# Performance work log

Hardware: AMD Instinct MI355X
Metric: run time of the kernel (lower is better)

## Reference

```python
import jax, jax.numpy as jnp
import numpy as np

B, T, K = 512, 1024, 48          # batch, seq_len, n_tokens
START, END = 46, 47              # token_dict['START'], token_dict['END']
NEG = -10000.0


def setup_inputs() -> dict:
    key = jax.random.key(0)
    k1, k2 = jax.random.split(key)
    feats = jax.random.normal(k1, (B, T, K), dtype=jnp.float32)
    transitions = jax.random.normal(k2, (K, K), dtype=jnp.float32)
    return {"feats": feats, "transitions": transitions}


def _mask_transitions(transitions):
    # Mirrors __init__: no transition out of END-column target / into START row.
    t = transitions.at[START, :].set(NEG)
    t = t.at[:, END].set(NEG)
    return t


def _crf_logz(feats, trans):
    """forward_prop: CRF forward algorithm. feats [T,K], trans [K_next,K_prev]."""
    init = jnp.full((K,), NEG, feats.dtype).at[START].set(0.0)

    def step(alpha, feat):
        # scores[next, prev] = alpha[prev] + trans[next, prev] + feat[next]
        scores = alpha[None, :] + trans + feat[:, None]
        return jax.nn.logsumexp(scores, axis=1), None

    alpha, _ = jax.lax.scan(step, init, feats)
    return jax.nn.logsumexp(alpha + trans[END])


def _viterbi(feats, trans):
    """viterbi_decode: max-product recurrence + backtrace. feats [T,K]."""
    init = jnp.full((K,), NEG, feats.dtype).at[START].set(0.0)

    def step(v, feat):
        # NOTE: original takes argmax BEFORE adding emission, then adds feat.
        scores = v[None, :] + trans          # [K_next, K_prev]
        bp = jnp.argmax(scores, axis=1)      # backpointers [K]
        return jnp.max(scores, axis=1) + feat, bp

    v, bptrs = jax.lax.scan(step, init, feats)   # bptrs [T, K]
    term = v + trans[END]
    last = jnp.argmax(term)
    path_score = term[last]

    def back(tag, bp):
        return bp[tag], tag

    _, path = jax.lax.scan(back, last, bptrs, reverse=True)  # path [T]
    return path_score, path


def reference(feats, transitions):
    trans = _mask_transitions(transitions)
    logz = jax.vmap(lambda f: _crf_logz(f, trans))(feats)          # [B]
    scores, paths = jax.vmap(lambda f: _viterbi(f, trans))(feats)  # [B], [B,T]
    return logz, scores, paths
```

## Files before the change

kernel.cpp:

```cpp
#include <hip/hip_runtime.h>

#define NB 512
#define NT 1024
#define NK 48
#define NEGV -10000.0f
#define S_START 46
#define S_END 47

__device__ __forceinline__ float rfl_f32(float x) {
    return __int_as_float(__builtin_amdgcn_readfirstlane(__float_as_int(x)));
}

extern "C" __global__ __launch_bounds__(128, 1)
void crf_fused(const float* __restrict__ feats, const float* __restrict__ trans,
               float* __restrict__ out)
{
    __shared__ unsigned char bp[NT * NK];
    __shared__ unsigned char comp[64 * NK];
    __shared__ unsigned char boundary[64];
    __shared__ float eabuf[64];
    __shared__ float vbuf[64];

    const int b = blockIdx.x;
    const int wave = threadIdx.x >> 6;
    const int lane = threadIdx.x & 63;
    const bool act = lane < NK;
    const int LL = act ? lane : (NK - 1);
    const float* f = feats + (size_t)b * NT * NK;
    const float* fb = f + LL;

    float tEnd = NEGV;
    if (act && lane != S_END) tEnd = trans[S_END * NK + lane];

    if (wave == 0) {
        float Erow[NK];
        {
            const bool rowdead = (lane == S_START);
            const float4* r4 = (const float4*)(trans + LL * NK);
            #pragma unroll
            for (int q = 0; q < NK / 4; ++q) {
                float4 r = r4[q];
                const int c = 4 * q;
                Erow[c + 0] = (rowdead || c + 0 == S_END) ? 0.0f : __expf(r.x);
                Erow[c + 1] = (rowdead || c + 1 == S_END) ? 0.0f : __expf(r.y);
                Erow[c + 2] = (rowdead || c + 2 == S_END) ? 0.0f : __expf(r.z);
                Erow[c + 3] = (rowdead || c + 3 == S_END) ? 0.0f : __expf(r.w);
            }
        }
        float u = (lane == S_START) ? 0.0f : NEGV;
        float Muni = 0.0f;
        eabuf[lane] = __expf(u);
        __builtin_amdgcn_wave_barrier();

        float fr0 = fb[0 * NK], fr1 = fb[1 * NK], fr2 = fb[2 * NK], fr3 = fb[3 * NK];

        auto fstep = [&](float fc) {
            float ea[NK];
            {
                const float4* e4 = (const float4*)eabuf;
                #pragma unroll
                for (int q = 0; q < NK / 4; ++q) {
                    float4 r = e4[q];
                    ea[4 * q + 0] = r.x; ea[4 * q + 1] = r.y;
                    ea[4 * q + 2] = r.z; ea[4 * q + 3] = r.w;
                }
            }
            float a0 = 0.f, a1 = 0.f, a2 = 0.f, a3 = 0.f;
            #pragma unroll
            for (int p = 0; p < NK; p += 4) {
                a0 = fmaf(Erow[p + 0], ea[p + 0], a0);
                a1 = fmaf(Erow[p + 1], ea[p + 1], a1);
                a2 = fmaf(Erow[p + 2], ea[p + 2], a2);
                a3 = fmaf(Erow[p + 3], ea[p + 3], a3);
            }
            float acc = (a0 + a1) + (a2 + a3);
            float w = __logf(acc) + fc;
            float dM = rfl_f32(w);
            Muni += dM;
            u = w - dM;
            __builtin_amdgcn_wave_barrier();
            eabuf[lane] = __expf(u);
            __builtin_amdgcn_wave_barrier();
        };

        for (int t = 0; t < NT; t += 4) {
            { float fc = fr0; int nr = (t + 4 < NT) ? t + 4 : NT - 1; fr0 = fb[nr * NK]; fstep(fc); }
            { float fc = fr1; int nr = (t + 5 < NT) ? t + 5 : NT - 1; fr1 = fb[nr * NK]; fstep(fc); }
            { float fc = fr2; int nr = (t + 6 < NT) ? t + 6 : NT - 1; fr2 = fb[nr * NK]; fstep(fc); }
            { float fc = fr3; int nr = (t + 7 < NT) ? t + 7 : NT - 1; fr3 = fb[nr * NK]; fstep(fc); }
        }
        float x = act ? (u + tEnd) : -INFINITY;
        float M2 = x;
        #pragma unroll
        for (int off = 32; off >= 1; off >>= 1)
            M2 = fmaxf(M2, __shfl_xor(M2, off, 64));
        float e = __expf(x - M2);
        #pragma unroll
        for (int off = 32; off >= 1; off >>= 1)
            e += __shfl_xor(e, off, 64);
        if (lane == 0) out[b] = Muni + M2 + __logf(e);
    } else {
        float trow[NK];
        {
            const bool rowdead = (lane == S_START);
            const float4* r4 = (const float4*)(trans + LL * NK);
            #pragma unroll
            for (int q = 0; q < NK / 4; ++q) {
                float4 r = r4[q];
                const int c = 4 * q;
                trow[c + 0] = (rowdead || c + 0 == S_END) ? NEGV : r.x;
                trow[c + 1] = (rowdead || c + 1 == S_END) ? NEGV : r.y;
                trow[c + 2] = (rowdead || c + 2 == S_END) ? NEGV : r.z;
                trow[c + 3] = (rowdead || c + 3 == S_END) ? NEGV : r.w;
            }
        }
        float v = (lane == S_START) ? 0.0f : NEGV;
        vbuf[lane] = v;
        __builtin_amdgcn_wave_barrier();

        float fr0 = fb[0 * NK], fr1 = fb[1 * NK], fr2 = fb[2 * NK], fr3 = fb[3 * NK];
        const int big = 63;

        auto vstep = [&](float fc, int tt) {
            float s[NK];
            {
                const float4* v4 = (const float4*)vbuf;
                #pragma unroll
                for (int q = 0; q < NK / 4; ++q) {
                    float4 r = v4[q];
                    s[4 * q + 0] = r.x + trow[4 * q + 0];
                    s[4 * q + 1] = r.y + trow[4 * q + 1];
                    s[4 * q + 2] = r.z + trow[4 * q + 2];
                    s[4 * q + 3] = r.w + trow[4 * q + 3];
                }
            }
            float m16[16];
            #pragma unroll
            for (int i = 0; i < 16; ++i)
                m16[i] = fmaxf(fmaxf(s[3 * i], s[3 * i + 1]), s[3 * i + 2]);
            float m6[6];
            #pragma unroll
            for (int i = 0; i < 5; ++i)
                m6[i] = fmaxf(fmaxf(m16[3 * i], m16[3 * i + 1]), m16[3 * i + 2]);
            m6[5] = m16[15];
            float best = fmaxf(fmaxf(fmaxf(m6[0], m6[1]), m6[2]),
                               fmaxf(fmaxf(m6[3], m6[4]), m6[5]));
            int ix[NK];
            #pragma unroll
            for (int p = 0; p < NK; ++p)
                ix[p] = (s[p] != best) ? big : p;
            int n16[16];
            #pragma unroll
            for (int i = 0; i < 16; ++i)
                n16[i] = min(min(ix[3 * i], ix[3 * i + 1]), ix[3 * i + 2]);
            int n6[6];
            #pragma unroll
            for (int i = 0; i < 5; ++i)
                n6[i] = min(min(n16[3 * i], n16[3 * i + 1]), n16[3 * i + 2]);
            n6[5] = n16[15];
            int bi = min(min(min(n6[0], n6[1]), n6[2]),
                         min(min(n6[3], n6[4]), n6[5]));

            bp[tt * NK + LL] = (unsigned char)bi;
            v = best + fc;
            __builtin_amdgcn_wave_barrier();
            vbuf[lane] = v;
            __builtin_amdgcn_wave_barrier();
        };

        for (int t = 0; t < NT; t += 4) {
            { float fc = fr0; int nr = (t + 4 < NT) ? t + 4 : NT - 1; fr0 = fb[nr * NK]; vstep(fc, t + 0); }
            { float fc = fr1; int nr = (t + 5 < NT) ? t + 5 : NT - 1; fr1 = fb[nr * NK]; vstep(fc, t + 1); }
            { float fc = fr2; int nr = (t + 6 < NT) ? t + 6 : NT - 1; fr2 = fb[nr * NK]; vstep(fc, t + 2); }
            { float fc = fr3; int nr = (t + 7 < NT) ? t + 7 : NT - 1; fr3 = fb[nr * NK]; vstep(fc, t + 3); }
        }
        float xv = act ? (v + tEnd) : -INFINITY;
        int idx = act ? lane : 63;
        float val = xv;
        #pragma unroll
        for (int off = 32; off >= 1; off >>= 1) {
            float ov = __shfl_xor(val, off, 64);
            int   oi = __shfl_xor(idx, off, 64);
            if (ov > val || (ov == val && oi < idx)) { val = ov; idx = oi; }
        }
        if (lane == 0) out[NB + b] = val;
        const int last = idx;

        __builtin_amdgcn_wave_barrier();
        int cur[NK];
        #pragma unroll
        for (int k = 0; k < NK; ++k) cur[k] = k;
        const int tbase = lane * 16;
        for (int i = 15; i >= 0; --i) {
            const int t = tbase + i;
            #pragma unroll
            for (int k = 0; k < NK; ++k) cur[k] = bp[t * NK + cur[k]];
        }
        #pragma unroll
        for (int k = 0; k < NK; ++k) comp[lane * NK + k] = (unsigned char)cur[k];
        __builtin_amdgcn_wave_barrier();

        if (lane == 0) {
            int tag = last;
            for (int l = 63; l >= 0; --l) {
                boundary[l] = (unsigned char)tag;
                tag = comp[l * NK + tag];
            }
        }
        __builtin_amdgcn_wave_barrier();

        int tag = boundary[lane];
        float* pout = out + 2 * NB + (size_t)b * NT;
        for (int i = 15; i >= 0; --i) {
            const int t = tbase + i;
            pout[t] = (float)tag;
            tag = bp[t * NK + tag];
        }
    }
}

extern "C" void kernel_launch(void* const* d_in, const int* in_sizes, int n_in,
                              void* d_out, int out_size, void* d_ws, size_t ws_size,
                              hipStream_t stream) {
    (void)in_sizes; (void)n_in; (void)d_ws; (void)ws_size; (void)out_size;
    const float* feats = (const float*)d_in[0];
    const float* trans = (const float*)d_in[1];
    float* out = (float*)d_out;
    crf_fused<<<dim3(NB), dim3(128), 0, stream>>>(feats, trans, out);
}
```

Before: 519.0 us.

## Split Viterbi into max-only sweep, parallel chunk recompute, and trace kernels

The sequential Viterbi sweep now computes only the running max, with no argmax, and checkpoints the score vector every 16 steps to workspace. A second kernel launched over (batch, chunk) recomputes backpointers for each chunk from its checkpoint in parallel and writes them, plus a composed chunk map, to global memory. A third kernel chains the chunk maps and backtraces the path. The goal is to shorten the serial critical path of the Viterbi wave, at the cost of extra launches and workspace traffic. The old fused kernel remains as a fallback when workspace is missing or too small.

```diff
diff --git a/kernel.cpp b/kernel.cpp
--- a/kernel.cpp
+++ b/kernel.cpp
@@ -6,18 +6,27 @@
 #define NEGV -10000.0f
 #define S_START 46
 #define S_END 47
+#define NCH 64
+#define CLEN 16
+
+#define WS_CKPT 0
+#define WS_CKPT_SZ (NB * NCH * NK * 4)
+#define WS_LAST (WS_CKPT + WS_CKPT_SZ)
+#define WS_LAST_SZ (NB * 4)
+#define WS_COMP (WS_LAST + WS_LAST_SZ)
+#define WS_COMP_SZ (NB * NCH * NK)
+#define WS_BP (WS_COMP + WS_COMP_SZ)
+#define WS_BP_SZ (NB * NCH * CLEN * NK)
+#define WS_NEED (WS_BP + WS_BP_SZ)
 
 __device__ __forceinline__ float rfl_f32(float x) {
     return __int_as_float(__builtin_amdgcn_readfirstlane(__float_as_int(x)));
 }
 
 extern "C" __global__ __launch_bounds__(128, 1)
-void crf_fused(const float* __restrict__ feats, const float* __restrict__ trans,
-               float* __restrict__ out)
+void crf_sweep(const float* __restrict__ feats, const float* __restrict__ trans,
+               float* __restrict__ out, unsigned char* __restrict__ ws)
 {
-    __shared__ unsigned char bp[NT * NK];
-    __shared__ unsigned char comp[64 * NK];
-    __shared__ unsigned char boundary[64];
     __shared__ float eabuf[64];
     __shared__ float vbuf[64];
 
@@ -117,9 +126,10 @@
         float v = (lane == S_START) ? 0.0f : NEGV;
         vbuf[lane] = v;
         __builtin_amdgcn_wave_barrier();
+        float* ckpt = (float*)(ws + WS_CKPT) + (size_t)b * NCH * NK;
+        if (act) ckpt[lane] = v;
 
         float fr0 = fb[0 * NK], fr1 = fb[1 * NK], fr2 = fb[2 * NK], fr3 = fb[3 * NK];
-        const int big = 63;
 
         auto vstep = [&](float fc, int tt) {
             float s[NK];
@@ -145,6 +155,309 @@
             m6[5] = m16[15];
             float best = fmaxf(fmaxf(fmaxf(m6[0], m6[1]), m6[2]),
                                fmaxf(fmaxf(m6[3], m6[4]), m6[5]));
+            v = best + fc;
+            __builtin_amdgcn_wave_barrier();
+            vbuf[lane] = v;
+            __builtin_amdgcn_wave_barrier();
+            if (((tt + 1) & (CLEN - 1)) == 0 && (tt + 1) < NT && act)
+                ckpt[((tt + 1) >> 4) * NK + lane] = v;
+        };
+
+        for (int t = 0; t < NT; t += 4) {
+            { float fc = fr0; int nr = (t + 4 < NT) ? t + 4 : NT - 1; fr0 = fb[nr * NK]; vstep(fc, t + 0); }
+            { float fc = fr1; int nr = (t + 5 < NT) ? t + 5 : NT - 1; fr1 = fb[nr * NK]; vstep(fc, t + 1); }
+            { float fc = fr2; int nr = (t + 6 < NT) ? t + 6 : NT - 1; fr2 = fb[nr * NK]; vstep(fc, t + 2); }
+            { float fc = fr3; int nr = (t + 7 < NT) ? t + 7 : NT - 1; fr3 = fb[nr * NK]; vstep(fc, t + 3); }
+        }
+        float xv = act ? (v + tEnd) : -INFINITY;
+        int idx = act ? lane : 63;
+        float val = xv;
+        #pragma unroll
+        for (int off = 32; off >= 1; off >>= 1) {
+            float ov = __shfl_xor(val, off, 64);
+            int   oi = __shfl_xor(idx, off, 64);
+            if (ov > val || (ov == val && oi < idx)) { val = ov; idx = oi; }
+        }
+        if (lane == 0) {
+            out[NB + b] = val;
+            ((int*)(ws + WS_LAST))[b] = idx;
+        }
+    }
+}
+
+extern "C" __global__ void
+crf_chunks(const float* __restrict__ feats, const float* __restrict__ trans,
+           unsigned char* __restrict__ ws)
+{
+    __shared__ float vbuf[64];
+    __shared__ unsigned char bp16[CLEN * NK];
+
+    const int b = blockIdx.x;
+    const int c = blockIdx.y;
+    const int lane = threadIdx.x & 63;
+    const bool act = lane < NK;
+    const int LL = act ? lane : (NK - 1);
+
+    float trow[NK];
+    {
+        const bool rowdead = (lane == S_START);
+        const float4* r4 = (const float4*)(trans + LL * NK);
+        #pragma unroll
+        for (int q = 0; q < NK / 4; ++q) {
+            float4 r = r4[q];
+            const int cc = 4 * q;
+            trow[cc + 0] = (rowdead || cc + 0 == S_END) ? NEGV : r.x;
+            trow[cc + 1] = (rowdead || cc + 1 == S_END) ? NEGV : r.y;
+            trow[cc + 2] = (rowdead || cc + 2 == S_END) ? NEGV : r.z;
+            trow[cc + 3] = (rowdead || cc + 3 == S_END) ? NEGV : r.w;
+        }
+    }
+    const float* ckpt = (const float*)(ws + WS_CKPT) + ((size_t)b * NCH + c) * NK;
+    if (act) vbuf[lane] = ckpt[lane];
+    __builtin_amdgcn_wave_barrier();
+
+    const float* fb = feats + (size_t)b * NT * NK + (size_t)c * CLEN * NK + LL;
+    const int big = 63;
+
+    float fr0 = fb[0 * NK], fr1 = fb[1 * NK], fr2 = fb[2 * NK], fr3 = fb[3 * NK];
+
+    auto vstepB = [&](float fc, int tt) {
+        float s[NK];
+        {
+            const float4* v4 = (const float4*)vbuf;
+            #pragma unroll
+            for (int q = 0; q < NK / 4; ++q) {
+                float4 r = v4[q];
+                s[4 * q + 0] = r.x + trow[4 * q + 0];
+                s[4 * q + 1] = r.y + trow[4 * q + 1];
+                s[4 * q + 2] = r.z + trow[4 * q + 2];
+                s[4 * q + 3] = r.w + trow[4 * q + 3];
+            }
+        }
+        float m16[16];
+        #pragma unroll
+        for (int i = 0; i < 16; ++i)
+            m16[i] = fmaxf(fmaxf(s[3 * i], s[3 * i + 1]), s[3 * i + 2]);
+        float m6[6];
+        #pragma unroll
+        for (int i = 0; i < 5; ++i)
+            m6[i] = fmaxf(fmaxf(m16[3 * i], m16[3 * i + 1]), m16[3 * i + 2]);
+        m6[5] = m16[15];
+        float best = fmaxf(fmaxf(fmaxf(m6[0], m6[1]), m6[2]),
+                           fmaxf(fmaxf(m6[3], m6[4]), m6[5]));
+        int ix[NK];
+        #pragma unroll
+        for (int p = 0; p < NK; ++p)
+            ix[p] = (s[p] != best) ? big : p;
+        int n16[16];
+        #pragma unroll
+        for (int i = 0; i < 16; ++i)
+            n16[i] = min(min(ix[3 * i], ix[3 * i + 1]), ix[3 * i + 2]);
+        int n6[6];
+        #pragma unroll
+        for (int i = 0; i < 5; ++i)
+            n6[i] = min(min(n16[3 * i], n16[3 * i + 1]), n16[3 * i + 2]);
+        n6[5] = n16[15];
+        int bi = min(min(min(n6[0], n6[1]), n6[2]),
+                     min(min(n6[3], n6[4]), n6[5]));
+
+        bp16[tt * NK + LL] = (unsigned char)bi;
+        float v = best + fc;
+        __builtin_amdgcn_wave_barrier();
+        vbuf[lane] = v;
+        __builtin_amdgcn_wave_barrier();
+    };
+
+    for (int t = 0; t < CLEN; t += 4) {
+        { float fc = fr0; int nr = (t + 4 < CLEN) ? t + 4 : CLEN - 1; fr0 = fb[nr * NK]; vstepB(fc, t + 0); }
+        { float fc = fr1; int nr = (t + 5 < CLEN) ? t + 5 : CLEN - 1; fr1 = fb[nr * NK]; vstepB(fc, t + 1); }
+        { float fc = fr2; int nr = (t + 6 < CLEN) ? t + 6 : CLEN - 1; fr2 = fb[nr * NK]; vstepB(fc, t + 2); }
+        { float fc = fr3; int nr = (t + 7 < CLEN) ? t + 7 : CLEN - 1; fr3 = fb[nr * NK]; vstepB(fc, t + 3); }
+    }
+    __builtin_amdgcn_wave_barrier();
+
+    {
+        unsigned int* dst = (unsigned int*)(ws + WS_BP) + ((size_t)b * NCH + c) * (CLEN * NK / 4);
+        const unsigned int* src = (const unsigned int*)bp16;
+        for (int j = lane; j < CLEN * NK / 4; j += 64) dst[j] = src[j];
+    }
+    if (act) {
+        int tag = lane;
+        #pragma unroll
+        for (int i = CLEN - 1; i >= 0; --i) tag = bp16[i * NK + tag];
+        (ws + WS_COMP)[((size_t)b * NCH + c) * NK + lane] = (unsigned char)tag;
+    }
+}
+
+extern "C" __global__ __launch_bounds__(64, 1)
+void crf_trace(float* __restrict__ out, unsigned char* __restrict__ ws)
+{
+    __shared__ unsigned char compL[NCH * NK];
+    __shared__ unsigned char boundary[NCH];
+
+    const int b = blockIdx.x;
+    const int lane = threadIdx.x & 63;
+
+    {
+        const unsigned int* src = (const unsigned int*)(ws + WS_COMP) + (size_t)b * (NCH * NK / 4);
+        unsigned int* dst = (unsigned int*)compL;
+        for (int j = lane; j < NCH * NK / 4; j += 64) dst[j] = src[j];
+    }
+    __builtin_amdgcn_wave_barrier();
+
+    if (lane == 0) {
+        int tag = ((const int*)(ws + WS_LAST))[b];
+        for (int l = NCH - 1; l >= 0; --l) {
+            boundary[l] = (unsigned char)tag;
+            tag = compL[l * NK + tag];
+        }
+    }
+    __builtin_amdgcn_wave_barrier();
+
+    int tag = boundary[lane];
+    const unsigned char* bpc = (ws + WS_BP) + ((size_t)b * NCH + lane) * (CLEN * NK);
+    float* pout = out + 2 * NB + (size_t)b * NT + lane * CLEN;
+    #pragma unroll
+    for (int i = CLEN - 1; i >= 0; --i) {
+        pout[i] = (float)tag;
+        tag = bpc[i * NK + tag];
+    }
+}
+
+extern "C" __global__ __launch_bounds__(128, 1)
+void crf_fused(const float* __restrict__ feats, const float* __restrict__ trans,
+               float* __restrict__ out)
+{
+    __shared__ unsigned char bp[NT * NK];
+    __shared__ unsigned char comp[64 * NK];
+    __shared__ unsigned char boundary[64];
+    __shared__ float eabuf[64];
+    __shared__ float vbuf[64];
+
+    const int b = blockIdx.x;
+    const int wave = threadIdx.x >> 6;
+    const int lane = threadIdx.x & 63;
+    const bool act = lane < NK;
+    const int LL = act ? lane : (NK - 1);
+    const float* f = feats + (size_t)b * NT * NK;
+    const float* fb = f + LL;
+
+    float tEnd = NEGV;
+    if (act && lane != S_END) tEnd = trans[S_END * NK + lane];
+
+    if (wave == 0) {
+        float Erow[NK];
+        {
+            const bool rowdead = (lane == S_START);
+            const float4* r4 = (const float4*)(trans + LL * NK);
+            #pragma unroll
+            for (int q = 0; q < NK / 4; ++q) {
+                float4 r = r4[q];
+                const int c = 4 * q;
+                Erow[c + 0] = (rowdead || c + 0 == S_END) ? 0.0f : __expf(r.x);
+                Erow[c + 1] = (rowdead || c + 1 == S_END) ? 0.0f : __expf(r.y);
+                Erow[c + 2] = (rowdead || c + 2 == S_END) ? 0.0f : __expf(r.z);
+                Erow[c + 3] = (rowdead || c + 3 == S_END) ? 0.0f : __expf(r.w);
+            }
+        }
+        float u = (lane == S_START) ? 0.0f : NEGV;
+        float Muni = 0.0f;
+        eabuf[lane] = __expf(u);
+        __builtin_amdgcn_wave_barrier();
+
+        float fr0 = fb[0 * NK], fr1 = fb[1 * NK], fr2 = fb[2 * NK], fr3 = fb[3 * NK];
+
+        auto fstep = [&](float fc) {
+            float ea[NK];
+            {
+                const float4* e4 = (const float4*)eabuf;
+                #pragma unroll
+                for (int q = 0; q < NK / 4; ++q) {
+                    float4 r = e4[q];
+                    ea[4 * q + 0] = r.x; ea[4 * q + 1] = r.y;
+                    ea[4 * q + 2] = r.z; ea[4 * q + 3] = r.w;
+                }
+            }
+            float a0 = 0.f, a1 = 0.f, a2 = 0.f, a3 = 0.f;
+            #pragma unroll
+            for (int p = 0; p < NK; p += 4) {
+                a0 = fmaf(Erow[p + 0], ea[p + 0], a0);
+                a1 = fmaf(Erow[p + 1], ea[p + 1], a1);
+                a2 = fmaf(Erow[p + 2], ea[p + 2], a2);
+                a3 = fmaf(Erow[p + 3], ea[p + 3], a3);
+            }
+            float acc = (a0 + a1) + (a2 + a3);
+            float w = __logf(acc) + fc;
+            float dM = rfl_f32(w);
+            Muni += dM;
+            u = w - dM;
+            __builtin_amdgcn_wave_barrier();
+            eabuf[lane] = __expf(u);
+            __builtin_amdgcn_wave_barrier();
+        };
+
+        for (int t = 0; t < NT; t += 4) {
+            { float fc = fr0; int nr = (t + 4 < NT) ? t + 4 : NT - 1; fr0 = fb[nr * NK]; fstep(fc); }
+            { float fc = fr1; int nr = (t + 5 < NT) ? t + 5 : NT - 1; fr1 = fb[nr * NK]; fstep(fc); }
+            { float fc = fr2; int nr = (t + 6 < NT) ? t + 6 : NT - 1; fr2 = fb[nr * NK]; fstep(fc); }
+            { float fc = fr3; int nr = (t + 7 < NT) ? t + 7 : NT - 1; fr3 = fb[nr * NK]; fstep(fc); }
+        }
+        float x = act ? (u + tEnd) : -INFINITY;
+        float M2 = x;
+        #pragma unroll
+        for (int off = 32; off >= 1; off >>= 1)
+            M2 = fmaxf(M2, __shfl_xor(M2, off, 64));
+        float e = __expf(x - M2);
+        #pragma unroll
+        for (int off = 32; off >= 1; off >>= 1)
+            e += __shfl_xor(e, off, 64);
+        if (lane == 0) out[b] = Muni + M2 + __logf(e);
+    } else {
+        float trow[NK];
+        {
+            const bool rowdead = (lane == S_START);
+            const float4* r4 = (const float4*)(trans + LL * NK);
+            #pragma unroll
+            for (int q = 0; q < NK / 4; ++q) {
+                float4 r = r4[q];
+                const int c = 4 * q;
+                trow[c + 0] = (rowdead || c + 0 == S_END) ? NEGV : r.x;
+                trow[c + 1] = (rowdead || c + 1 == S_END) ? NEGV : r.y;
+                trow[c + 2] = (rowdead || c + 2 == S_END) ? NEGV : r.z;
+                trow[c + 3] = (rowdead || c + 3 == S_END) ? NEGV : r.w;
+            }
+        }
+        float v = (lane == S_START) ? 0.0f : NEGV;
+        vbuf[lane] = v;
+        __builtin_amdgcn_wave_barrier();
+
+        float fr0 = fb[0 * NK], fr1 = fb[1 * NK], fr2 = fb[2 * NK], fr3 = fb[3 * NK];
+        const int big = 63;
+
+        auto vstep = [&](float fc, int tt) {
+            float s[NK];
+            {
+                const float4* v4 = (const float4*)vbuf;
+                #pragma unroll
+                for (int q = 0; q < NK / 4; ++q) {
+                    float4 r = v4[q];
+                    s[4 * q + 0] = r.x + trow[4 * q + 0];
+                    s[4 * q + 1] = r.y + trow[4 * q + 1];
+                    s[4 * q + 2] = r.z + trow[4 * q + 2];
+                    s[4 * q + 3] = r.w + trow[4 * q + 3];
+                }
+            }
+            float m16[16];
+            #pragma unroll
+            for (int i = 0; i < 16; ++i)
+                m16[i] = fmaxf(fmaxf(s[3 * i], s[3 * i + 1]), s[3 * i + 2]);
+            float m6[6];
+            #pragma unroll
+            for (int i = 0; i < 5; ++i)
+                m6[i] = fmaxf(fmaxf(m16[3 * i], m16[3 * i + 1]), m16[3 * i + 2]);
+            m6[5] = m16[15];
+            float best = fmaxf(fmaxf(fmaxf(m6[0], m6[1]), m6[2]),
+                               fmaxf(fmaxf(m6[3], m6[4]), m6[5]));
             int ix[NK];
             #pragma unroll
             for (int p = 0; p < NK; ++p)
@@ -222,9 +535,16 @@
 extern "C" void kernel_launch(void* const* d_in, const int* in_sizes, int n_in,
                               void* d_out, int out_size, void* d_ws, size_t ws_size,
                               hipStream_t stream) {
-    (void)in_sizes; (void)n_in; (void)d_ws; (void)ws_size; (void)out_size;
+    (void)in_sizes; (void)n_in; (void)out_size;
     const float* feats = (const float*)d_in[0];
     const float* trans = (const float*)d_in[1];
     float* out = (float*)d_out;
-    crf_fused<<<dim3(NB), dim3(128), 0, stream>>>(feats, trans, out);
+    if (d_ws != nullptr && ws_size >= (size_t)WS_NEED) {
+        unsigned char* ws = (unsigned char*)d_ws;
+        crf_sweep<<<dim3(NB), dim3(128), 0, stream>>>(feats, trans, out, ws);
+        crf_chunks<<<dim3(NB, NCH), dim3(64), 0, stream>>>(feats, trans, ws);
+        crf_trace<<<dim3(NB), dim3(64), 0, stream>>>(out, ws);
+    } else {
+        crf_fused<<<dim3(NB), dim3(128), 0, stream>>>(feats, trans, out);
+    }
 }
```

Result: slower. 586.2 us (+13.0%).
